# Optimization experiments

Hardware: AMD Instinct MI355X
Metric: run time of the kernel (lower is better)

The kernel has to match this reference:

```python
import jax, jax.numpy as jnp
import numpy as np

SCALE = 64.0
MARGIN = 0.35
LAMBDA = 0.4
GAMMA = 2
EPS = 1e-12


def _l2_normalize(v, axis=-1):
    n = jnp.sqrt(jnp.sum(v * v, axis=axis, keepdims=True))
    return v / jnp.maximum(n, EPS)


def setup_inputs() -> dict:
    key = jax.random.key(0)
    k1, k2, k3, k4 = jax.random.split(key, 4)
    B, D, C = 1024, 512, 100000
    stdv = 1.0 / np.sqrt(D)
    x = jax.random.normal(k1, (B, D), dtype=jnp.float32)
    target = jax.random.randint(k2, (B,), 0, C, dtype=jnp.int64)
    id_agent = jax.random.uniform(k3, (C, D), dtype=jnp.float32, minval=-stdv, maxval=stdv)
    b = jax.random.uniform(k4, (C, D), dtype=jnp.float32, minval=-stdv, maxval=stdv)
    return {"x": x, "target": target, "id_agent": id_agent, "b": b}


def reference(x, target, id_agent, b):
    B = x.shape[0]
    x_n = _l2_normalize(x, axis=1)              # [B, D]
    w = _l2_normalize(id_agent, axis=1)         # [C, D] (in-place normalize in torch)

    # discriminative loss
    w_batch = w[target]                          # [B, D] gather
    d = x_n - w_batch                            # displacement vectors
    bt = b[target]                               # [B, D]
    bt_norm = jnp.sqrt(jnp.sum(bt * bt, axis=1, keepdims=True))
    bt_norm_c = jnp.clip(bt_norm, 0.0, 0.05)
    bt_unit = bt / jnp.maximum(bt_norm, EPS)
    resid = d - bt_unit * bt_norm_c
    loss_disc = jnp.mean(jnp.sqrt(jnp.sum(resid * resid, axis=1)))

    # AM-softmax logits with margin on target class (training mode)
    score = x_n @ w.T                            # [B, C] large GEMM
    rows = jnp.arange(B)
    score = score.at[rows, target].add(-MARGIN)
    score = score * SCALE

    # focal cross-entropy: CE mean first, then focal modulation (as in source)
    logsm = jax.nn.log_softmax(score, axis=1)
    nll = -logsm[rows, target]
    logp = jnp.mean(nll)
    p = jnp.exp(-logp)
    loss_score = (1.0 - p) ** GAMMA * logp

    return (LAMBDA * loss_disc + loss_score)[None]  # shape [1]
```

## Files before the change

### kernel.cpp

```cpp
#include <hip/hip_runtime.h>
#include <hip/hip_bf16.h>

typedef __attribute__((ext_vector_type(4))) int i32x4;
typedef __attribute__((ext_vector_type(16))) int i32x16;

#define B_N 1024
#define D_K 512
#define C_N 100000
#define SCALE_F 64.0f
#define MARGIN_F 0.35f
#define BM 128
#define BN 128
#define BKB 128
#define NT_ 782
#define MT_ 8
#define MAXL 64.0f
#define KQ (SCALE_F / (127.0f * 127.0f))

__device__ __forceinline__ float dot4(float4 a, float4 b) {
    return a.x * b.x + a.y * b.y + a.z * b.z + a.w * b.w;
}
__device__ __forceinline__ float amax4(float4 a) {
    return fmaxf(fmaxf(fabsf(a.x), fabsf(a.y)), fmaxf(fabsf(a.z), fabsf(a.w)));
}
__device__ __forceinline__ int packq(float v0, float v1, float v2, float v3, float qs) {
    int q0 = __float2int_rn(v0 * qs), q1 = __float2int_rn(v1 * qs);
    int q2 = __float2int_rn(v2 * qs), q3 = __float2int_rn(v3 * qs);
    return (q0 & 0xFF) | ((q1 & 0xFF) << 8) | ((q2 & 0xFF) << 16) | ((q3 & 0xFF) << 24);
}

__global__ void normx_disc_kernel(const float* __restrict__ x,
                                  const int* __restrict__ target,
                                  const float* __restrict__ ida,
                                  const float* __restrict__ bmat,
                                  char* __restrict__ xq,
                                  float* __restrict__ sx,
                                  float* __restrict__ dpart,
                                  float* __restrict__ tlogit,
                                  float* __restrict__ rowsum) {
    int row = blockIdx.x * 4 + (threadIdx.x >> 6);
    int l = threadIdx.x & 63;
    long t = (long)target[row];
    const float4* xp = (const float4*)(x + (size_t)row * D_K);
    const float4* wp = (const float4*)(ida + (size_t)t * D_K);
    const float4* bp = (const float4*)(bmat + (size_t)t * D_K);
    float4 x0 = xp[l], x1 = xp[64 + l];
    float4 w0 = wp[l], w1 = wp[64 + l];
    float4 b0 = bp[l], b1 = bp[64 + l];
    float xssq = dot4(x0, x0) + dot4(x1, x1);
    float wssq = dot4(w0, w0) + dot4(w1, w1);
    float bssq = dot4(b0, b0) + dot4(b1, b1);
    float xmx = fmaxf(amax4(x0), amax4(x1));
#pragma unroll
    for (int m = 1; m < 64; m <<= 1) {
        xssq += __shfl_xor(xssq, m);
        wssq += __shfl_xor(wssq, m);
        bssq += __shfl_xor(bssq, m);
        xmx = fmaxf(xmx, __shfl_xor(xmx, m));
    }
    float xinv = 1.0f / fmaxf(sqrtf(xssq), 1e-12f);
    float winv = 1.0f / fmaxf(sqrtf(wssq), 1e-12f);
    float btn = sqrtf(bssq);
    float cs = fminf(btn, 0.05f) / fmaxf(btn, 1e-12f);

    float sxm = fmaxf(xmx * xinv, 1e-12f);
    float qs = 127.0f / sxm * xinv;
    int* oq = (int*)(xq + (size_t)row * D_K);
    oq[l] = packq(x0.x, x0.y, x0.z, x0.w, qs);
    oq[64 + l] = packq(x1.x, x1.y, x1.z, x1.w, qs);

    float xs[8] = {x0.x, x0.y, x0.z, x0.w, x1.x, x1.y, x1.z, x1.w};
    float wv[8] = {w0.x, w0.y, w0.z, w0.w, w1.x, w1.y, w1.z, w1.w};
    float bv[8] = {b0.x, b0.y, b0.z, b0.w, b1.x, b1.y, b1.z, b1.w};
    float rss = 0.0f, dt = 0.0f;
#pragma unroll
    for (int i = 0; i < 8; ++i) {
        float xn = xs[i] * xinv;
        float wn = wv[i] * winv;
        float d = xn - wn;
        float r = d - bv[i] * cs;
        rss += r * r;
        dt += xn * wn;
    }
#pragma unroll
    for (int m = 1; m < 64; m <<= 1) {
        rss += __shfl_xor(rss, m);
        dt += __shfl_xor(dt, m);
    }
    if (l == 0) {
        sx[row] = sxm;
        dpart[row] = sqrtf(rss);
        tlogit[row] = SCALE_F * dt;
        rowsum[row] = 0.0f;
    }
}

__global__ void norm_w_kernel(const float* __restrict__ w,
                              char* __restrict__ wq,
                              float* __restrict__ sw) {
    int row = blockIdx.x * 4 + (threadIdx.x >> 6);
    int l = threadIdx.x & 63;
    const float4* rp = (const float4*)(w + (size_t)row * D_K);
    float4 a = rp[l], b = rp[64 + l];
    float ssq = dot4(a, a) + dot4(b, b);
    float mx = fmaxf(amax4(a), amax4(b));
#pragma unroll
    for (int m = 1; m < 64; m <<= 1) {
        ssq += __shfl_xor(ssq, m);
        mx = fmaxf(mx, __shfl_xor(mx, m));
    }
    float inv = 1.0f / fmaxf(sqrtf(ssq), 1e-12f);
    float swm = fmaxf(mx * inv, 1e-12f);
    float qs = 127.0f / swm * inv;
    int* oq = (int*)(wq + (size_t)row * D_K);
    oq[l] = packq(a.x, a.y, a.z, a.w, qs);
    oq[64 + l] = packq(b.x, b.y, b.z, b.w, qs);
    if (l == 0) sw[row] = swm;
}

__global__ __launch_bounds__(256, 4) void gemm_lse_kernel(const char* __restrict__ A,
                                                          const char* __restrict__ W,
                                                          const float* __restrict__ sx,
                                                          const float* __restrict__ sw,
                                                          float* __restrict__ rowsum) {
    __shared__ char As[BM * BKB];
    __shared__ char Bs[BN * BKB];
    __shared__ float sxl[BM];
    __shared__ float swl[BN];
    __shared__ float rs[2][BM];

    int tid = threadIdx.x;
    int wave = tid >> 6, l = tid & 63;
    int wm = wave >> 1, wn = wave & 1;

    int tile = (blockIdx.x & 7) * NT_ + (blockIdx.x >> 3);
    int nt = tile >> 3, mt = tile & 7;
    int m0 = mt * BM, n0 = nt * BN;

    int srow = l >> 3;
    int scolB = ((l & 7) ^ (l >> 3)) * 16;

    if (tid < BM) {
        sxl[tid] = sx[m0 + tid];
        int c = n0 + tid;
        swl[tid] = sw[c < C_N ? c : C_N - 1];
    }

    i32x16 acc[2][2];
#pragma unroll
    for (int i = 0; i < 2; ++i)
#pragma unroll
        for (int j = 0; j < 2; ++j)
#pragma unroll
            for (int e = 0; e < 16; ++e) acc[i][j][e] = 0;

    int l31 = l & 31, hi5 = l >> 5;

    for (int kt = 0; kt < 4; ++kt) {
#pragma unroll
        for (int i = 0; i < 4; ++i) {
            int rb = wave * 32 + i * 8;
            const char* ga = A + (size_t)(m0 + rb + srow) * D_K + kt * BKB + scolB;
            __builtin_amdgcn_global_load_lds(
                (const __attribute__((address_space(1))) void*)ga,
                (__attribute__((address_space(3))) void*)&As[rb * BKB], 16, 0, 0);
            int rn = n0 + rb + srow;
            rn = rn < C_N ? rn : C_N - 1;
            const char* gb = W + (size_t)rn * D_K + kt * BKB + scolB;
            __builtin_amdgcn_global_load_lds(
                (const __attribute__((address_space(1))) void*)gb,
                (__attribute__((address_space(3))) void*)&Bs[rb * BKB], 16, 0, 0);
        }
        __syncthreads();

#pragma unroll
        for (int ks = 0; ks < 4; ++ks) {
            int px = (((ks << 1) | hi5) ^ (l & 7)) * 16;
            i32x4 af[2], bfr[2];
#pragma unroll
            for (int mi = 0; mi < 2; ++mi)
                af[mi] = *(const i32x4*)&As[(wm * 64 + mi * 32 + l31) * BKB + px];
#pragma unroll
            for (int ni = 0; ni < 2; ++ni)
                bfr[ni] = *(const i32x4*)&Bs[(wn * 64 + ni * 32 + l31) * BKB + px];
#pragma unroll
            for (int mi = 0; mi < 2; ++mi)
#pragma unroll
                for (int ni = 0; ni < 2; ++ni)
                    acc[mi][ni] = __builtin_amdgcn_mfma_i32_32x32x32_i8(af[mi], bfr[ni], acc[mi][ni], 0, 0, 0);
        }
        __syncthreads();
    }

    float fcv[2];
#pragma unroll
    for (int ni = 0; ni < 2; ++ni)
        fcv[ni] = swl[wn * 64 + ni * 32 + l31];
    bool cok[2];
#pragma unroll
    for (int ni = 0; ni < 2; ++ni)
        cok[ni] = (n0 + wn * 64 + ni * 32 + l31) < C_N;

#pragma unroll
    for (int mi = 0; mi < 2; ++mi) {
#pragma unroll
        for (int reg = 0; reg < 16; ++reg) {
            int rloc = mi * 32 + (reg & 3) + 8 * (reg >> 2) + 4 * hi5;
            float fr = sxl[wm * 64 + rloc] * KQ;
            float se = 0.0f;
#pragma unroll
            for (int ni = 0; ni < 2; ++ni)
                if (cok[ni]) se += __expf((float)acc[mi][ni][reg] * fr * fcv[ni] - MAXL);
#pragma unroll
            for (int xm = 1; xm < 32; xm <<= 1) se += __shfl_xor(se, xm);
            if (l31 == 0) rs[wn][wm * 64 + rloc] = se;
        }
    }
    __syncthreads();
    if (tid < BM) {
        float s = rs[0][tid] + rs[1][tid];
        atomicAdd(&rowsum[m0 + tid], s);
    }
}

__global__ void rowfin_final_kernel(const float* __restrict__ rowsum,
                                    const float* __restrict__ tlogit,
                                    const float* __restrict__ dpart,
                                    float* __restrict__ out) {
    __shared__ float redn[16];
    __shared__ float redd[16];
    int tid = threadIdx.x;
    float lse = MAXL + logf(rowsum[tid]);
    float st = tlogit[tid];
    float corr = __expf(st - lse) * (__expf(-SCALE_F * MARGIN_F) - 1.0f);
    float lse2 = lse + log1pf(corr);
    float nll = lse2 - (st - SCALE_F * MARGIN_F);
    float dv = dpart[tid];
#pragma unroll
    for (int xm = 1; xm < 64; xm <<= 1) {
        nll += __shfl_xor(nll, xm);
        dv += __shfl_xor(dv, xm);
    }
    if ((tid & 63) == 0) {
        redn[tid >> 6] = nll;
        redd[tid >> 6] = dv;
    }
    __syncthreads();
    if (tid == 0) {
        float sn = 0.0f, sd = 0.0f;
#pragma unroll
        for (int i = 0; i < 16; ++i) { sn += redn[i]; sd += redd[i]; }
        float logp = sn * (1.0f / B_N);
        float disc = sd * (1.0f / B_N);
        float p = __expf(-logp);
        float om = 1.0f - p;
        out[0] = 0.4f * disc + om * om * logp;
    }
}

extern "C" void kernel_launch(void* const* d_in, const int* in_sizes, int n_in,
                              void* d_out, int out_size, void* d_ws, size_t ws_size,
                              hipStream_t stream) {
    const float* x = (const float*)d_in[0];
    const int* target = (const int*)d_in[1];
    const float* ida = (const float*)d_in[2];
    const float* bmat = (const float*)d_in[3];
    float* out = (float*)d_out;

    char* ws = (char*)d_ws;
    size_t off = 0;
    float* rowsum = (float*)(ws + off);  off += (size_t)B_N * 4;
    char* xq = (char*)(ws + off);        off += (size_t)B_N * D_K;
    char* wq = (char*)(ws + off);        off += (size_t)C_N * D_K;
    float* sx = (float*)(ws + off);      off += (size_t)B_N * 4;
    float* sw = (float*)(ws + off);      off += (size_t)C_N * 4;
    float* tlogit = (float*)(ws + off);  off += (size_t)B_N * 4;
    float* dpart = (float*)(ws + off);   off += (size_t)B_N * 4;

    normx_disc_kernel<<<B_N / 4, 256, 0, stream>>>(x, target, ida, bmat, xq, sx, dpart, tlogit, rowsum);
    norm_w_kernel<<<C_N / 4, 256, 0, stream>>>(ida, wq, sw);
    gemm_lse_kernel<<<MT_ * NT_, 256, 0, stream>>>(xq, wq, sx, sw, rowsum);
    rowfin_final_kernel<<<1, 1024, 0, stream>>>(rowsum, tlogit, dpart, out);
}
```

Baseline: 163.3 us.

## Widen GEMM N-tile to 256 and switch to 16x16x64 int8 MFMA

Doubles the class-dimension tile per workgroup from 128 to 256, so each wave computes a 64x128 sub-tile. The int8 GEMM now uses the 16x16x64 MFMA with 4x8 accumulators instead of 2x2 32x32x32 accumulators. The exp-sum epilogue is remapped to the new accumulator layout, and its cross-lane reduction now spans 16 lanes instead of 32. The aim is more reuse of each A tile, fewer blocks, and fewer shuffles per row. In exchange, register and LDS use per block rise, and launch bounds drop to 2 blocks per CU, which lowers occupancy.

```diff
diff --git a/kernel.cpp b/kernel.cpp
--- a/kernel.cpp
+++ b/kernel.cpp
@@ -2,7 +2,6 @@
 #include <hip/hip_bf16.h>
 
 typedef __attribute__((ext_vector_type(4))) int i32x4;
-typedef __attribute__((ext_vector_type(16))) int i32x16;
 
 #define B_N 1024
 #define D_K 512
@@ -10,9 +9,9 @@
 #define SCALE_F 64.0f
 #define MARGIN_F 0.35f
 #define BM 128
-#define BN 128
+#define BN 256
 #define BKB 128
-#define NT_ 782
+#define NT_ 391
 #define MT_ 8
 #define MAXL 64.0f
 #define KQ (SCALE_F / (127.0f * 127.0f))
@@ -118,7 +117,7 @@
     if (l == 0) sw[row] = swm;
 }
 
-__global__ __launch_bounds__(256, 4) void gemm_lse_kernel(const char* __restrict__ A,
+__global__ __launch_bounds__(256, 2) void gemm_lse_kernel(const char* __restrict__ A,
                                                           const char* __restrict__ W,
                                                           const float* __restrict__ sx,
                                                           const float* __restrict__ sw,
@@ -133,28 +132,26 @@
     int wave = tid >> 6, l = tid & 63;
     int wm = wave >> 1, wn = wave & 1;
 
-    int tile = (blockIdx.x & 7) * NT_ + (blockIdx.x >> 3);
-    int nt = tile >> 3, mt = tile & 7;
+    int wgid = (blockIdx.x & 7) * NT_ + (blockIdx.x >> 3);
+    int nt = wgid >> 3, mt = wgid & 7;
     int m0 = mt * BM, n0 = nt * BN;
 
     int srow = l >> 3;
     int scolB = ((l & 7) ^ (l >> 3)) * 16;
 
-    if (tid < BM) {
-        sxl[tid] = sx[m0 + tid];
+    {
         int c = n0 + tid;
         swl[tid] = sw[c < C_N ? c : C_N - 1];
-    }
-
-    i32x16 acc[2][2];
-#pragma unroll
-    for (int i = 0; i < 2; ++i)
-#pragma unroll
-        for (int j = 0; j < 2; ++j)
-#pragma unroll
-            for (int e = 0; e < 16; ++e) acc[i][j][e] = 0;
-
-    int l31 = l & 31, hi5 = l >> 5;
+        if (tid < BM) sxl[tid] = sx[m0 + tid];
+    }
+
+    i32x4 acc[4][8];
+#pragma unroll
+    for (int i = 0; i < 4; ++i)
+#pragma unroll
+        for (int j = 0; j < 8; ++j) acc[i][j] = (i32x4){0, 0, 0, 0};
+
+    int cl = l & 15, hi = l >> 4;
 
     for (int kt = 0; kt < 4; ++kt) {
 #pragma unroll
@@ -164,6 +161,10 @@
             __builtin_amdgcn_global_load_lds(
                 (const __attribute__((address_space(1))) void*)ga,
                 (__attribute__((address_space(3))) void*)&As[rb * BKB], 16, 0, 0);
+        }
+#pragma unroll
+        for (int i = 0; i < 8; ++i) {
+            int rb = wave * 64 + i * 8;
             int rn = n0 + rb + srow;
             rn = rn < C_N ? rn : C_N - 1;
             const char* gb = W + (size_t)rn * D_K + kt * BKB + scolB;
@@ -174,46 +175,44 @@
         __syncthreads();
 
 #pragma unroll
-        for (int ks = 0; ks < 4; ++ks) {
-            int px = (((ks << 1) | hi5) ^ (l & 7)) * 16;
-            i32x4 af[2], bfr[2];
-#pragma unroll
-            for (int mi = 0; mi < 2; ++mi)
-                af[mi] = *(const i32x4*)&As[(wm * 64 + mi * 32 + l31) * BKB + px];
-#pragma unroll
-            for (int ni = 0; ni < 2; ++ni)
-                bfr[ni] = *(const i32x4*)&Bs[(wn * 64 + ni * 32 + l31) * BKB + px];
-#pragma unroll
-            for (int mi = 0; mi < 2; ++mi)
-#pragma unroll
-                for (int ni = 0; ni < 2; ++ni)
-                    acc[mi][ni] = __builtin_amdgcn_mfma_i32_32x32x32_i8(af[mi], bfr[ni], acc[mi][ni], 0, 0, 0);
+        for (int kk = 0; kk < 2; ++kk) {
+            int px = (((kk << 2) | hi) ^ (cl & 7)) * 16;
+            i32x4 af[4], bfr[8];
+#pragma unroll
+            for (int mi = 0; mi < 4; ++mi)
+                af[mi] = *(const i32x4*)&As[(wm * 64 + mi * 16 + cl) * BKB + px];
+#pragma unroll
+            for (int ni = 0; ni < 8; ++ni)
+                bfr[ni] = *(const i32x4*)&Bs[(wn * 128 + ni * 16 + cl) * BKB + px];
+#pragma unroll
+            for (int mi = 0; mi < 4; ++mi)
+#pragma unroll
+                for (int ni = 0; ni < 8; ++ni)
+                    acc[mi][ni] = __builtin_amdgcn_mfma_i32_16x16x64_i8(af[mi], bfr[ni], acc[mi][ni], 0, 0, 0);
         }
         __syncthreads();
     }
 
-    float fcv[2];
-#pragma unroll
-    for (int ni = 0; ni < 2; ++ni)
-        fcv[ni] = swl[wn * 64 + ni * 32 + l31];
-    bool cok[2];
-#pragma unroll
-    for (int ni = 0; ni < 2; ++ni)
-        cok[ni] = (n0 + wn * 64 + ni * 32 + l31) < C_N;
-
-#pragma unroll
-    for (int mi = 0; mi < 2; ++mi) {
-#pragma unroll
-        for (int reg = 0; reg < 16; ++reg) {
-            int rloc = mi * 32 + (reg & 3) + 8 * (reg >> 2) + 4 * hi5;
-            float fr = sxl[wm * 64 + rloc] * KQ;
+    float fcv[8];
+    bool cok[8];
+#pragma unroll
+    for (int ni = 0; ni < 8; ++ni) {
+        fcv[ni] = swl[wn * 128 + ni * 16 + cl];
+        cok[ni] = (n0 + wn * 128 + ni * 16 + cl) < C_N;
+    }
+
+#pragma unroll
+    for (int mi = 0; mi < 4; ++mi) {
+#pragma unroll
+        for (int j = 0; j < 4; ++j) {
+            float fr = sxl[wm * 64 + mi * 16 + hi * 4 + j] * KQ;
             float se = 0.0f;
 #pragma unroll
-            for (int ni = 0; ni < 2; ++ni)
-                if (cok[ni]) se += __expf((float)acc[mi][ni][reg] * fr * fcv[ni] - MAXL);
-#pragma unroll
-            for (int xm = 1; xm < 32; xm <<= 1) se += __shfl_xor(se, xm);
-            if (l31 == 0) rs[wn][wm * 64 + rloc] = se;
+            for (int ni = 0; ni < 8; ++ni)
+                if (cok[ni]) se += __expf((float)acc[mi][ni][j] * fr * fcv[ni] - MAXL);
+#pragma unroll
+            for (int xm = 1; xm < 16; xm <<= 1) se += __shfl_xor(se, xm);
+            if (cl == 0) rs[wn][wm * 64 + mi * 16 + hi * 4 + j] = se;
         }
     }
     __syncthreads();
```

Result: faster. 139.5 us (-14.6%).
